# Kernel optimization log

Measured on AMD Instinct MI355X. Metric: run time of the kernel, lower is better.

The kernel has to match this reference:

```python
import jax, jax.numpy as jnp
import numpy as np

B, T, I, H, HID, NT = 1024, 200, 64, 512, 256, 1


def setup_inputs() -> dict:
    key = jax.random.key(0)
    ks = jax.random.split(key, 12)
    s_h = 1.0 / np.sqrt(H)
    s_i = 1.0 / np.sqrt(I)
    s_hid = 1.0 / np.sqrt(HID)
    return {
        "x": jax.random.normal(ks[0], (B, T, I), dtype=jnp.float32),
        "timestamps": jax.random.uniform(ks[1], (B, T), dtype=jnp.float32),
        # TimeLSTM params: W_all: Linear(H -> 4H), U_all: Linear(I -> 4H), W_d: Linear(H -> H)
        "W_all": jax.random.uniform(ks[2], (4 * H, H), minval=-s_h, maxval=s_h, dtype=jnp.float32),
        "b_all": jax.random.uniform(ks[3], (4 * H,), minval=-s_h, maxval=s_h, dtype=jnp.float32),
        "U_all": jax.random.uniform(ks[4], (4 * H, I), minval=-s_i, maxval=s_i, dtype=jnp.float32),
        "b_u": jax.random.uniform(ks[5], (4 * H,), minval=-s_i, maxval=s_i, dtype=jnp.float32),
        "W_d": jax.random.uniform(ks[6], (H, H), minval=-s_h, maxval=s_h, dtype=jnp.float32),
        "b_d": jax.random.uniform(ks[7], (H,), minval=-s_h, maxval=s_h, dtype=jnp.float32),
        # MLP head: Linear(H -> HID), ReLU, Linear(HID -> NT); dropout in eval mode (identity)
        "W1": jax.random.uniform(ks[8], (HID, H), minval=-s_h, maxval=s_h, dtype=jnp.float32),
        "b1": jax.random.uniform(ks[9], (HID,), minval=-s_h, maxval=s_h, dtype=jnp.float32),
        "W2": jax.random.uniform(ks[10], (NT, HID), minval=-s_hid, maxval=s_hid, dtype=jnp.float32),
        "b2": jax.random.uniform(ks[11], (NT,), minval=-s_hid, maxval=s_hid, dtype=jnp.float32),
    }


def _time_lstm_last_h(x, timestamps, W_all, b_all, U_all, b_u, W_d, b_d):
    # x: [B, T, I], timestamps: [B, T]. Returns final hidden state h_T: [B, H].
    # Precompute input projections for all steps: [T, B, 4H]
    xg = jnp.einsum('bti,gi->tbg', x, U_all) + b_u
    ts = timestamps.T  # [T, B]

    def step(carry, inp):
        h, c = carry
        xgt, tt = inp  # [B, 4H], [B]
        c_s1 = jnp.tanh(c @ W_d.T + b_d)                 # short-term memory
        c_adj = c - c_s1 + c_s1 * tt[:, None]            # time-discounted cell
        gates = h @ W_all.T + b_all + xgt                # [B, 4H]
        f, i, o, c_tmp = jnp.split(jax.nn.sigmoid(gates), 4, axis=1)
        c_new = f * c_adj + i * c_tmp
        h_new = o * jnp.tanh(c_new)
        return (h_new, c_new), None

    h0 = jnp.zeros((x.shape[0], W_d.shape[0]), dtype=x.dtype)
    (h_last, _), _ = jax.lax.scan(step, (h0, h0), (xg, ts))
    return h_last


def reference(x, timestamps, W_all, b_all, U_all, b_u, W_d, b_d, W1, b1, W2, b2):
    h = _time_lstm_last_h(x, timestamps, W_all, b_all, U_all, b_u, W_d, b_d)
    # MLP head (dropout = identity in eval): Linear -> ReLU -> Linear; classification=False so no sigmoid
    hidden = jax.nn.relu(h @ W1.T + b1)
    return hidden @ W2.T + b2  # [B, NT]
```

## Files before the change

kernel.cpp:

```cpp
#include <hip/hip_runtime.h>
#include <cstdint>
#include <cstddef>

#define B_   1024
#define T_   200
#define I_   64
#define H_   512
#define HID_ 256
#define LDA_ 1088
#define NFRAG 88
#define NBUF 12
#define RINV 8

typedef __bf16 bf16;
typedef __bf16 bf16x4 __attribute__((ext_vector_type(4)));
typedef __bf16 bf16x8 __attribute__((ext_vector_type(8)));
typedef float  f32x4  __attribute__((ext_vector_type(4)));

__device__ inline void gload_lds16(const bf16* g, void* l) {
  void* gg = (void*)g;
  __builtin_amdgcn_global_load_lds((__attribute__((address_space(1))) void*)gg,
                                   (__attribute__((address_space(3))) void*)l,
                                   16, 0, 0);
}

__device__ inline float sigm(float x) { return 1.f / (1.f + __expf(-x)); }
__device__ inline float tanh_f(float x) {
  float e = __expf(2.f * fabsf(x));
  float r = 1.f - 2.f / (e + 1.f);
  return copysignf(r, x);
}
__device__ inline uint32_t bf16bits(float v) {
  union { bf16 h; unsigned short u; } cv; cv.h = (bf16)v; return (uint32_t)cv.u;
}

__global__ __launch_bounds__(512, 2)
void persist(bf16* __restrict__ states,
             const float* __restrict__ x, const float* __restrict__ tsT,
             const bf16* __restrict__ img,
             const float* __restrict__ ba, const float* __restrict__ bu,
             const float* __restrict__ bd, int* __restrict__ flags)
{
  __shared__ __align__(16) bf16 Wl[NFRAG * 512];

  const int tid = threadIdx.x;
  const int l   = tid & 63, w = tid >> 6;
  const int bid = blockIdx.x;
  const int mt  = bid & 7, jt = bid >> 3;
  const int m0  = mt * 128;
  const int col = l & 15, kh = l >> 4;
  const size_t SB = (size_t)B_ * LDA_;

  {
    const bf16* src = img + (size_t)jt * (NFRAG * 512);
#pragma unroll
    for (int it = 0; it < 11; ++it)
      gload_lds16(src + it * 4096 + tid * 8, (char*)Wl + it * 8192 + tid * 16);
  }

  float bg[4], bdv;
#pragma unroll
  for (int g = 0; g < 4; ++g) {
    int n = g * 512 + jt * 16 + col;
    bg[g] = ba[n] + bu[n];
  }
  bdv = bd[jt * 16 + col];
  __syncthreads();

  float cst[4] = {0.f, 0.f, 0.f, 0.f};
  const bf16x8* Wf = (const bf16x8*)Wl;

  int cur = 0, nxt = 1;
  for (int t = 0; t < T_; ++t) {
    const bf16* Ac = states + (size_t)cur * SB;
    bf16*       An = states + (size_t)nxt * SB;

    const int rb = m0 + w * 16 + kh * 4;
    float4 tt4 = *(const float4*)(tsT + (size_t)t * B_ + rb);
    const bool dox = (tid < 64) && (t + 1 < T_);
    const int xr = m0 + jt * 4 + (tid >> 4), xc = (tid & 15) * 4;
    float4 xv = {0.f, 0.f, 0.f, 0.f};
    if (dox) xv = *(const float4*)(x + ((size_t)xr * T_ + (t + 1)) * I_ + xc);

    if (t > 0) {
      if (w == 0) {
        int* fl = flags + mt * 32 + (l & 31);
        while (__hip_atomic_load(fl, __ATOMIC_RELAXED,
                                 __HIP_MEMORY_SCOPE_AGENT) < t)
          __builtin_amdgcn_s_sleep(1);
        if ((t & (RINV - 1)) == 0)
          __builtin_amdgcn_fence(__ATOMIC_ACQUIRE, "agent");
        asm volatile("" ::: "memory");
      }
      __syncthreads();
    }

    const size_t ra = (size_t)(m0 + w * 16 + col) * LDA_ + kh * 8;

    bf16x8 areg[34];
#pragma unroll
    for (int kk = 0; kk < 18; ++kk)
      areg[kk] = *(const bf16x8*)(Ac + ra + kk * 32);
#pragma unroll
    for (int kk = 0; kk < 16; ++kk)
      areg[18 + kk] = *(const bf16x8*)(Ac + ra + 576 + kk * 32);

    f32x4 acc[4], accd0, accd1;
#pragma unroll
    for (int g = 0; g < 4; ++g) acc[g] = (f32x4){bg[g], bg[g], bg[g], bg[g]};
    accd0 = (f32x4){bdv, bdv, bdv, bdv};
    accd1 = (f32x4){0.f, 0.f, 0.f, 0.f};

#pragma unroll
    for (int kk = 0; kk < 18; ++kk) {
#pragma unroll
      for (int g = 0; g < 4; ++g) {
        bf16x8 bv = Wf[(g * 18 + kk) * 64 + l];
        acc[g] = __builtin_amdgcn_mfma_f32_16x16x32_bf16(areg[kk], bv, acc[g], 0, 0, 0);
      }
    }
#pragma unroll
    for (int kk = 0; kk < 16; kk += 2) {
      accd0 = __builtin_amdgcn_mfma_f32_16x16x32_bf16(areg[18 + kk],     Wf[(72 + kk) * 64 + l], accd0, 0, 0, 0);
      accd1 = __builtin_amdgcn_mfma_f32_16x16x32_bf16(areg[18 + kk + 1], Wf[(73 + kk) * 64 + l], accd1, 0, 0, 0);
    }

#pragma unroll
    for (int q = 0; q < 4; ++q) {
      int row   = rb + q;
      float tt  = (&tt4.x)[q];
      float cs1 = tanh_f(accd0[q] + accd1[q]);
      float cadj = cst[q] - cs1 + cs1 * tt;
      float fg = sigm(acc[0][q]);
      float ig = sigm(acc[1][q]);
      float og = sigm(acc[2][q]);
      float cg_ = sigm(acc[3][q]);
      float cn = fg * cadj + ig * cg_;
      float hn = og * tanh_f(cn);
      cst[q] = cn;

      uint32_t hb = bf16bits(hn), cb = bf16bits(cn);
      uint32_t hb2 = (uint32_t)__shfl_xor((int)hb, 1, 64);
      uint32_t cb2 = (uint32_t)__shfl_xor((int)cb, 1, 64);
      if ((l & 1) == 0) {
        uint32_t hwd = hb | (hb2 << 16);
        uint32_t cwd = cb | (cb2 << 16);
        uint32_t* hp = (uint32_t*)(An + (size_t)row * LDA_ + jt * 16 + col);
        uint32_t* cp = (uint32_t*)(An + (size_t)row * LDA_ + 576 + jt * 16 + col);
        __hip_atomic_store(hp, hwd, __ATOMIC_RELAXED, __HIP_MEMORY_SCOPE_AGENT);
        __hip_atomic_store(cp, cwd, __ATOMIC_RELAXED, __HIP_MEMORY_SCOPE_AGENT);
      }
    }
    if (dox) {
      union { bf16 h[4]; unsigned long long u; } pk;
      pk.h[0] = (bf16)xv.x; pk.h[1] = (bf16)xv.y;
      pk.h[2] = (bf16)xv.z; pk.h[3] = (bf16)xv.w;
      unsigned long long* xp =
          (unsigned long long*)(An + (size_t)xr * LDA_ + 512 + xc);
      __hip_atomic_store(xp, pk.u, __ATOMIC_RELAXED, __HIP_MEMORY_SCOPE_AGENT);
    }

    if (t + 1 < T_) {
      __syncthreads();
      if (tid == 0)
        __hip_atomic_store(flags + mt * 32 + jt, t + 1, __ATOMIC_RELAXED,
                           __HIP_MEMORY_SCOPE_AGENT);
    }

    cur = nxt;
    nxt = (nxt + 1 == NBUF) ? 0 : nxt + 1;
  }
}

__global__ void pack_wimg(const float* __restrict__ Wa, const float* __restrict__ Ua,
                          const float* __restrict__ Wd, bf16* __restrict__ img)
{
  int tid = blockIdx.x * 256 + threadIdx.x;
  if (tid >= 32 * NFRAG * 64) return;
  int l  = tid & 63;
  int f  = (tid >> 6) % NFRAG;
  int jt = tid / (NFRAG * 64);
  int col = l & 15, kh = l >> 4;
  float v[8];
  if (f < 72) {
    int g = f / 18, kk = f % 18;
    int n = g * 512 + jt * 16 + col;
    if (kk < 16) {
      int k = kk * 32 + kh * 8;
#pragma unroll
      for (int r = 0; r < 8; ++r) v[r] = Wa[(size_t)n * 512 + k + r];
    } else {
      int k = (kk - 16) * 32 + kh * 8;
#pragma unroll
      for (int r = 0; r < 8; ++r) v[r] = Ua[(size_t)n * 64 + k + r];
    }
  } else {
    int kk = f - 72;
    int n = jt * 16 + col;
    int k = kk * 32 + kh * 8;
#pragma unroll
    for (int r = 0; r < 8; ++r) v[r] = Wd[(size_t)n * 512 + k + r];
  }
  bf16* dst = img + (size_t)tid * 8;
#pragma unroll
  for (int r = 0; r < 8; ++r) dst[r] = (bf16)v[r];
}

__global__ void pack_w1(const float* __restrict__ W1, bf16* __restrict__ W1b)
{
  int idx = blockIdx.x * 256 + threadIdx.x;
  if (idx < HID_ * H_) W1b[idx] = (bf16)W1[idx];
}

__global__ void init_state(const float* __restrict__ x, const float* __restrict__ ts,
                           bf16* __restrict__ states, float* __restrict__ tsT,
                           int* __restrict__ flags)
{
  int idx = blockIdx.x * 256 + threadIdx.x;
  if (idx < 8 * 32) flags[idx] = 0;
  if (idx < B_ * T_) {
    int b = idx / T_, t = idx - b * T_;
    tsT[(size_t)t * B_ + b] = ts[idx];
  }
  if (idx >= B_ * LDA_) return;
  int b = idx / LDA_, k = idx - b * LDA_;
  bf16 v = (bf16)0.f;
  if (k >= 512 && k < 576)
    v = (bf16)x[(size_t)b * T_ * I_ + (k - 512)];
  states[idx] = v;
}

__global__ __launch_bounds__(256)
void gemm_bf16(const bf16* __restrict__ A, int lda,
               const bf16* __restrict__ W, int ldw,
               float* __restrict__ C, int ldc,
               const float* __restrict__ bias,
               int nsplit, int kb0, int ke0, int kb1, int ke1)
{
  __shared__ __align__(16) bf16 As[128 * 64];
  __shared__ __align__(16) bf16 Bs[128 * 64];

  const int tid  = threadIdx.x;
  const int lane = tid & 63;
  const int wave = tid >> 6;
  const int m0 = blockIdx.y * 128;
  const int n0 = blockIdx.x * 128;
  const int kb = (n0 < nsplit) ? kb0 : kb1;
  const int ke = (n0 < nsplit) ? ke0 : ke1;

  int aoff[4], boff[4];
#pragma unroll
  for (int r = 0; r < 4; ++r) {
    int o16 = r * 256 + tid;
    int row = o16 >> 3;
    int sp  = o16 & 7;
    int s   = sp ^ (row & 7);
    aoff[r] = row * lda + s * 8;
    boff[r] = row * ldw + s * 8;
  }

  f32x4 acc[4][4];
#pragma unroll
  for (int i = 0; i < 4; ++i)
#pragma unroll
    for (int j = 0; j < 4; ++j) acc[i][j] = (f32x4){0.f, 0.f, 0.f, 0.f};

  const int wm = wave >> 1, wn = wave & 1;
  const int r15 = lane & 15, khalf = lane >> 4, sw = lane & 7;

  for (int kt = kb; kt < ke; kt += 64) {
    const bf16* Ag = A + (size_t)m0 * lda + kt;
    const bf16* Wg = W + (size_t)n0 * ldw + kt;
#pragma unroll
    for (int r = 0; r < 4; ++r) {
      char* la = (char*)As + (size_t)(r * 256 + wave * 64) * 16;
      char* lb = (char*)Bs + (size_t)(r * 256 + wave * 64) * 16;
      gload_lds16(Ag + aoff[r], la);
      gload_lds16(Wg + boff[r], lb);
    }
    __syncthreads();

    const bf16x8* Ald = (const bf16x8*)As;
    const bf16x8* Bld = (const bf16x8*)Bs;
#pragma unroll
    for (int kk = 0; kk < 2; ++kk) {
      bf16x8 av[4], bv[4];
#pragma unroll
      for (int i = 0; i < 4; ++i) {
        int ra = wm * 64 + i * 16 + r15;
        av[i] = Ald[ra * 8 + ((kk * 4 + khalf) ^ sw)];
        int rbw = wn * 64 + i * 16 + r15;
        bv[i] = Bld[rbw * 8 + ((kk * 4 + khalf) ^ sw)];
      }
#pragma unroll
      for (int i = 0; i < 4; ++i)
#pragma unroll
        for (int j = 0; j < 4; ++j)
          acc[i][j] = __builtin_amdgcn_mfma_f32_16x16x32_bf16(av[i], bv[j], acc[i][j], 0, 0, 0);
    }
    __syncthreads();
  }

#pragma unroll
  for (int j = 0; j < 4; ++j) {
    int colc = n0 + wn * 64 + j * 16 + r15;
    float bb = bias[colc];
#pragma unroll
    for (int i = 0; i < 4; ++i) {
      int rbase = m0 + wm * 64 + i * 16 + khalf * 4;
#pragma unroll
      for (int q = 0; q < 4; ++q)
        C[(size_t)(rbase + q) * ldc + colc] = acc[i][j][q] + bb;
    }
  }
}

__global__ void mlp_out(const float* __restrict__ Gm, const float* __restrict__ W2,
                        const float* __restrict__ b2, float* __restrict__ out)
{
  int b = blockIdx.x, l = threadIdx.x;
  float s = 0.f;
#pragma unroll
  for (int k = l; k < HID_; k += 64)
    s += fmaxf(Gm[(size_t)b * HID_ + k], 0.f) * W2[k];
#pragma unroll
  for (int off = 32; off; off >>= 1) s += __shfl_xor(s, off, 64);
  if (l == 0) out[b] = s + b2[0];
}

extern "C" void kernel_launch(void* const* d_in, const int* in_sizes, int n_in,
                              void* d_out, int out_size, void* d_ws, size_t ws_size,
                              hipStream_t stream)
{
  const float* x  = (const float*)d_in[0];
  const float* ts = (const float*)d_in[1];
  const float* Wa = (const float*)d_in[2];
  const float* ba = (const float*)d_in[3];
  const float* Ua = (const float*)d_in[4];
  const float* bu = (const float*)d_in[5];
  const float* Wd = (const float*)d_in[6];
  const float* bd = (const float*)d_in[7];
  const float* W1 = (const float*)d_in[8];
  const float* b1 = (const float*)d_in[9];
  const float* W2 = (const float*)d_in[10];
  const float* b2 = (const float*)d_in[11];

  char* ws = (char*)d_ws;
  size_t o = 0;
  auto alloc = [&](size_t bytes) {
    size_t p = o;
    o += (bytes + 255) & ~(size_t)255;
    return p;
  };
  const size_t SB = (size_t)B_ * LDA_;
  bf16*  Wimg   = (bf16*) (ws + alloc((size_t)32 * NFRAG * 512 * 2));
  bf16*  W1b    = (bf16*) (ws + alloc((size_t)HID_ * H_ * 2));
  bf16*  states = (bf16*) (ws + alloc(SB * NBUF * 2));
  float* G      = (float*)(ws + alloc((size_t)B_ * HID_ * 4));
  float* tsT    = (float*)(ws + alloc((size_t)B_ * T_ * 4));
  int*   flags  = (int*)  (ws + alloc((size_t)8 * 32 * 4));

  pack_wimg<<<(32 * NFRAG * 64 + 255) / 256, 256, 0, stream>>>(Wa, Ua, Wd, Wimg);
  pack_w1<<<(HID_ * H_ + 255) / 256, 256, 0, stream>>>(W1, W1b);
  init_state<<<(B_ * LDA_ + 255) / 256, 256, 0, stream>>>(x, ts, states, tsT, flags);

  void* args[] = {(void*)&states, (void*)&x, (void*)&tsT,
                  (void*)&Wimg, (void*)&ba, (void*)&bu, (void*)&bd, (void*)&flags};
  hipLaunchCooperativeKernel((void*)persist, dim3(256), dim3(512), args, 0, stream);

  gemm_bf16<<<dim3(HID_ / 128, B_ / 128), 256, 0, stream>>>(
      states + 8 * SB, LDA_, W1b, H_, G, HID_, b1, 1 << 30, 0, 512, 0, 512);
  mlp_out<<<B_, 64, 0, stream>>>(G, W2, b2, (float*)d_out);
}
```

Measured before the change: 2.045 ms.

## Use per-wave flags and read x directly instead of staging in state buffer

Result: slower. 4.453 ms (+117.8%).

```diff
diff --git a/kernel.cpp b/kernel.cpp
--- a/kernel.cpp
+++ b/kernel.cpp
@@ -7,13 +7,12 @@
 #define I_   64
 #define H_   512
 #define HID_ 256
-#define LDA_ 1088
+#define LDA_ 1024
 #define NFRAG 88
 #define NBUF 12
 #define RINV 8
 
 typedef __bf16 bf16;
-typedef __bf16 bf16x4 __attribute__((ext_vector_type(4)));
 typedef __bf16 bf16x8 __attribute__((ext_vector_type(8)));
 typedef float  f32x4  __attribute__((ext_vector_type(4)));
 
@@ -50,6 +49,7 @@
   const int m0  = mt * 128;
   const int col = l & 15, kh = l >> 4;
   const size_t SB = (size_t)B_ * LDA_;
+  const int fbase = (mt * 8 + w) * 32;
 
   {
     const bf16* src = img + (size_t)jt * (NFRAG * 512);
@@ -77,33 +77,42 @@
 
     const int rb = m0 + w * 16 + kh * 4;
     float4 tt4 = *(const float4*)(tsT + (size_t)t * B_ + rb);
-    const bool dox = (tid < 64) && (t + 1 < T_);
-    const int xr = m0 + jt * 4 + (tid >> 4), xc = (tid & 15) * 4;
-    float4 xv = {0.f, 0.f, 0.f, 0.f};
-    if (dox) xv = *(const float4*)(x + ((size_t)xr * T_ + (t + 1)) * I_ + xc);
+    bf16x8 ax0, ax1;
+    {
+      const float* xp = x + ((size_t)(m0 + w * 16 + col) * T_ + t) * I_ + kh * 8;
+      float4 a0 = *(const float4*)(xp);
+      float4 a1 = *(const float4*)(xp + 4);
+      float4 b0 = *(const float4*)(xp + 32);
+      float4 b1 = *(const float4*)(xp + 36);
+      ax0 = (bf16x8){(bf16)a0.x, (bf16)a0.y, (bf16)a0.z, (bf16)a0.w,
+                     (bf16)a1.x, (bf16)a1.y, (bf16)a1.z, (bf16)a1.w};
+      ax1 = (bf16x8){(bf16)b0.x, (bf16)b0.y, (bf16)b0.z, (bf16)b0.w,
+                     (bf16)b1.x, (bf16)b1.y, (bf16)b1.z, (bf16)b1.w};
+    }
 
     if (t > 0) {
-      if (w == 0) {
-        int* fl = flags + mt * 32 + (l & 31);
-        while (__hip_atomic_load(fl, __ATOMIC_RELAXED,
-                                 __HIP_MEMORY_SCOPE_AGENT) < t)
-          __builtin_amdgcn_s_sleep(1);
-        if ((t & (RINV - 1)) == 0)
+      int* fl = flags + fbase + (l & 31);
+      while (__hip_atomic_load(fl, __ATOMIC_RELAXED,
+                               __HIP_MEMORY_SCOPE_AGENT) < t)
+        __builtin_amdgcn_s_sleep(1);
+      asm volatile("" ::: "memory");
+      if ((t & (RINV - 1)) == 0) {
+        __syncthreads();
+        if (tid == 0)
           __builtin_amdgcn_fence(__ATOMIC_ACQUIRE, "agent");
-        asm volatile("" ::: "memory");
+        __syncthreads();
       }
-      __syncthreads();
     }
 
     const size_t ra = (size_t)(m0 + w * 16 + col) * LDA_ + kh * 8;
 
-    bf16x8 areg[34];
-#pragma unroll
-    for (int kk = 0; kk < 18; ++kk)
+    bf16x8 areg[32];
+#pragma unroll
+    for (int kk = 0; kk < 16; ++kk)
       areg[kk] = *(const bf16x8*)(Ac + ra + kk * 32);
 #pragma unroll
     for (int kk = 0; kk < 16; ++kk)
-      areg[18 + kk] = *(const bf16x8*)(Ac + ra + 576 + kk * 32);
+      areg[16 + kk] = *(const bf16x8*)(Ac + ra + 512 + kk * 32);
 
     f32x4 acc[4], accd0, accd1;
 #pragma unroll
@@ -113,16 +122,17 @@
 
 #pragma unroll
     for (int kk = 0; kk < 18; ++kk) {
+      bf16x8 a = (kk < 16) ? areg[kk] : (kk == 16 ? ax0 : ax1);
 #pragma unroll
       for (int g = 0; g < 4; ++g) {
         bf16x8 bv = Wf[(g * 18 + kk) * 64 + l];
-        acc[g] = __builtin_amdgcn_mfma_f32_16x16x32_bf16(areg[kk], bv, acc[g], 0, 0, 0);
+        acc[g] = __builtin_amdgcn_mfma_f32_16x16x32_bf16(a, bv, acc[g], 0, 0, 0);
       }
     }
 #pragma unroll
     for (int kk = 0; kk < 16; kk += 2) {
-      accd0 = __builtin_amdgcn_mfma_f32_16x16x32_bf16(areg[18 + kk],     Wf[(72 + kk) * 64 + l], accd0, 0, 0, 0);
-      accd1 = __builtin_amdgcn_mfma_f32_16x16x32_bf16(areg[18 + kk + 1], Wf[(73 + kk) * 64 + l], accd1, 0, 0, 0);
+      accd0 = __builtin_amdgcn_mfma_f32_16x16x32_bf16(areg[16 + kk],     Wf[(72 + kk) * 64 + l], accd0, 0, 0, 0);
+      accd1 = __builtin_amdgcn_mfma_f32_16x16x32_bf16(areg[16 + kk + 1], Wf[(73 + kk) * 64 + l], accd1, 0, 0, 0);
     }
 
 #pragma unroll
@@ -146,24 +156,16 @@
         uint32_t hwd = hb | (hb2 << 16);
         uint32_t cwd = cb | (cb2 << 16);
         uint32_t* hp = (uint32_t*)(An + (size_t)row * LDA_ + jt * 16 + col);
-        uint32_t* cp = (uint32_t*)(An + (size_t)row * LDA_ + 576 + jt * 16 + col);
+        uint32_t* cp = (uint32_t*)(An + (size_t)row * LDA_ + 512 + jt * 16 + col);
         __hip_atomic_store(hp, hwd, __ATOMIC_RELAXED, __HIP_MEMORY_SCOPE_AGENT);
         __hip_atomic_store(cp, cwd, __ATOMIC_RELAXED, __HIP_MEMORY_SCOPE_AGENT);
       }
     }
-    if (dox) {
-      union { bf16 h[4]; unsigned long long u; } pk;
-      pk.h[0] = (bf16)xv.x; pk.h[1] = (bf16)xv.y;
-      pk.h[2] = (bf16)xv.z; pk.h[3] = (bf16)xv.w;
-      unsigned long long* xp =
-          (unsigned long long*)(An + (size_t)xr * LDA_ + 512 + xc);
-      __hip_atomic_store(xp, pk.u, __ATOMIC_RELAXED, __HIP_MEMORY_SCOPE_AGENT);
-    }
 
     if (t + 1 < T_) {
-      __syncthreads();
-      if (tid == 0)
-        __hip_atomic_store(flags + mt * 32 + jt, t + 1, __ATOMIC_RELAXED,
+      asm volatile("s_waitcnt vmcnt(0)" ::: "memory");
+      if (l == 0)
+        __hip_atomic_store(flags + fbase + jt, t + 1, __ATOMIC_RELAXED,
                            __HIP_MEMORY_SCOPE_AGENT);
     }
 
@@ -217,17 +219,13 @@
                            int* __restrict__ flags)
 {
   int idx = blockIdx.x * 256 + threadIdx.x;
-  if (idx < 8 * 32) flags[idx] = 0;
+  if (idx < 8 * 8 * 32) flags[idx] = 0;
   if (idx < B_ * T_) {
     int b = idx / T_, t = idx - b * T_;
     tsT[(size_t)t * B_ + b] = ts[idx];
   }
   if (idx >= B_ * LDA_) return;
-  int b = idx / LDA_, k = idx - b * LDA_;
-  bf16 v = (bf16)0.f;
-  if (k >= 512 && k < 576)
-    v = (bf16)x[(size_t)b * T_ * I_ + (k - 512)];
-  states[idx] = v;
+  states[idx] = (bf16)0.f;
 }
 
 __global__ __launch_bounds__(256)
@@ -358,7 +356,7 @@
   bf16*  states = (bf16*) (ws + alloc(SB * NBUF * 2));
   float* G      = (float*)(ws + alloc((size_t)B_ * HID_ * 4));
   float* tsT    = (float*)(ws + alloc((size_t)B_ * T_ * 4));
-  int*   flags  = (int*)  (ws + alloc((size_t)8 * 32 * 4));
+  int*   flags  = (int*)  (ws + alloc((size_t)8 * 8 * 32 * 4));
 
   pack_wimg<<<(32 * NFRAG * 64 + 255) / 256, 256, 0, stream>>>(Wa, Ua, Wd, Wimg);
   pack_w1<<<(HID_ * H_ + 255) / 256, 256, 0, stream>>>(W1, W1b);
```
